# Optimization experiments

Hardware: AMD Instinct MI355X
Metric: run time of the kernel (lower is better)

The kernel has to match this reference:

```python
import jax, jax.numpy as jnp
import numpy as np

N_NODES = 50000
NEG_SLOPE = 0.2

def _gat_conv(x, W, att_src, att_dst, bias, src, dst):
    # x: [N, in_c] -> h: [N, out_c]
    h = x @ W
    a_src = (h * att_src).sum(-1)  # [N]
    a_dst = (h * att_dst).sum(-1)  # [N]
    e = a_src[src] + a_dst[dst]    # [E]
    e = jnp.where(e > 0, e, NEG_SLOPE * e)  # LeakyReLU
    # segment softmax over destination node neighborhoods
    emax = jax.ops.segment_max(e, dst, num_segments=N_NODES)
    ee = jnp.exp(e - emax[dst])
    denom = jax.ops.segment_sum(ee, dst, num_segments=N_NODES)
    alpha = ee / denom[dst]        # [E]
    out = jax.ops.segment_sum(h[src] * alpha[:, None], dst, num_segments=N_NODES)
    return out + bias

def _with_self_loops(edge_index):
    # PyG GATConv default add_self_loops=True
    loop = jnp.arange(N_NODES, dtype=edge_index.dtype)
    src = jnp.concatenate([edge_index[0], loop])
    dst = jnp.concatenate([edge_index[1], loop])
    return src, dst

def setup_inputs() -> dict:
    key = jax.random.key(0)
    ks = jax.random.split(key, 11)
    in_c, hid_c, out_c = 256, 128, 64
    E = 800000
    x = jax.random.normal(ks[0], (N_NODES, in_c), dtype=jnp.float32)
    edge_index = jax.random.randint(ks[1], (2, E), 0, N_NODES, dtype=jnp.int64)
    s1 = 1.0 / np.sqrt(in_c)
    s2 = 1.0 / np.sqrt(hid_c)
    return {
        "x": x,
        "edge_index": edge_index,
        "W1": jax.random.normal(ks[2], (in_c, hid_c), dtype=jnp.float32) * s1,
        "att_src1": jax.random.normal(ks[3], (hid_c,), dtype=jnp.float32) * s2,
        "att_dst1": jax.random.normal(ks[4], (hid_c,), dtype=jnp.float32) * s2,
        "b1": jax.random.normal(ks[5], (hid_c,), dtype=jnp.float32) * 0.01,
        "W2": jax.random.normal(ks[6], (hid_c, out_c), dtype=jnp.float32) * s2,
        "att_src2": jax.random.normal(ks[7], (out_c,), dtype=jnp.float32) * (1.0 / np.sqrt(out_c)),
        "att_dst2": jax.random.normal(ks[8], (out_c,), dtype=jnp.float32) * (1.0 / np.sqrt(out_c)),
        "b2": jax.random.normal(ks[9], (out_c,), dtype=jnp.float32) * 0.01,
    }

def reference(x, edge_index, W1, att_src1, att_dst1, b1, W2, att_src2, att_dst2, b2):
    src, dst = _with_self_loops(edge_index)
    hid = _gat_conv(x, W1, att_src1, att_dst1, b1, src, dst)
    hid = jax.nn.relu(hid)
    out = _gat_conv(hid, W2, att_src2, att_dst2, b2, src, dst)
    return jax.nn.log_softmax(out, axis=1)
```

## Files before the change

kernel.cpp:

```cpp
#include <hip/hip_runtime.h>
#include <hip/hip_bf16.h>
#include <math.h>

#define N_NODES 50000
#define E_RAW   800000
#define E_TOT   850000
#define NEG_SLOPE 0.2f
#define CAP 64

#define NBKT   196
#define BCAP   5376
#define SCHUNK 4096
#define SB     208

typedef __attribute__((ext_vector_type(8))) short short8;
typedef __attribute__((ext_vector_type(4))) float f32x4;

__device__ __forceinline__ short f2bf(float f) {
    __hip_bfloat16 h = __float2bfloat16(f);
    return *reinterpret_cast<short*>(&h);
}
__device__ __forceinline__ unsigned int f2bfu(float f) {
    __hip_bfloat16 h = __float2bfloat16(f);
    return (unsigned int)*reinterpret_cast<unsigned short*>(&h);
}
__device__ __forceinline__ float bflo(unsigned int u) {
    return __uint_as_float(u << 16);
}
__device__ __forceinline__ float bfhi(unsigned int u) {
    return __uint_as_float(u & 0xffff0000u);
}

template<int K, int N>
__global__ __launch_bounds__(256) void gat_wf_kernel(
        const float* __restrict__ W, short* __restrict__ Wf) {
    constexpr int NT = N / 16;
    const int idx = blockIdx.x * 256 + threadIdx.x;
    if (idx >= K * N) return;
    const int j  = idx & 7;
    const int n  = (idx >> 3) & 15;
    const int q  = (idx >> 7) & 3;
    const int t  = (idx >> 9) % NT;
    const int kc = idx / (512 * NT);
    const int k   = kc * 32 + q * 8 + j;
    const int col = t * 16 + n;
    Wf[idx] = f2bf(W[(size_t)k * N + col]);
}

template<int K, int N, bool BF16_IN>
__device__ __forceinline__ void gemm_att_body(
        const int blk,
        const float* __restrict__ xf, const short* __restrict__ xb,
        const short* __restrict__ Wf,
        const float* __restrict__ att_src, const float* __restrict__ att_dst,
        short* __restrict__ h_bf,
        float* __restrict__ a_src, float* __restrict__ a_dst) {
    constexpr int NT = N / 16;
    constexpr int KC = K / 32;
    const int tid  = threadIdx.x;
    const int lane = tid & 63;
    const int wv   = tid >> 6;
    const int mrow = lane & 15;
    const int q    = lane >> 4;

    const int row0 = blk * 64 + wv * 16;
    const int rowA = row0 + mrow;
    const int rowAc = rowA < N_NODES ? rowA : 0;

    f32x4 acc[NT];
    #pragma unroll
    for (int t = 0; t < NT; ++t) acc[t] = f32x4{0.f, 0.f, 0.f, 0.f};

    #pragma unroll
    for (int kc = 0; kc < KC; ++kc) {
        short8 a;
        if (BF16_IN) {
            a = *(const short8*)&xb[(size_t)rowAc * K + kc * 32 + q * 8];
        } else {
            const float4 f0 = *(const float4*)&xf[(size_t)rowAc * K + kc * 32 + q * 8];
            const float4 f1 = *(const float4*)&xf[(size_t)rowAc * K + kc * 32 + q * 8 + 4];
            a[0] = f2bf(f0.x); a[1] = f2bf(f0.y); a[2] = f2bf(f0.z); a[3] = f2bf(f0.w);
            a[4] = f2bf(f1.x); a[5] = f2bf(f1.y); a[6] = f2bf(f1.z); a[7] = f2bf(f1.w);
        }
        #pragma unroll
        for (int t = 0; t < NT; ++t) {
            const short8 b = *(const short8*)&Wf[((size_t)(kc * NT + t) * 64 + lane) * 8];
            acc[t] = __builtin_amdgcn_mfma_f32_16x16x32_bf16(a, b, acc[t], 0, 0, 0);
        }
    }

    #pragma unroll
    for (int r = 0; r < 4; ++r) {
        const int rowD = row0 + q * 4 + r;
        float ps = 0.0f, pd = 0.0f;
        #pragma unroll
        for (int t = 0; t < NT; ++t) {
            const int col = t * 16 + mrow;
            ps = fmaf(acc[t][r], att_src[col], ps);
            pd = fmaf(acc[t][r], att_dst[col], pd);
        }
        #pragma unroll
        for (int off = 8; off > 0; off >>= 1) {
            ps += __shfl_xor(ps, off);
            pd += __shfl_xor(pd, off);
        }
        if (rowD < N_NODES) {
            if (mrow == 0) { a_src[rowD] = ps; a_dst[rowD] = pd; }
            #pragma unroll
            for (int t = 0; t < NT; ++t)
                h_bf[(size_t)rowD * N + t * 16 + mrow] = f2bf(acc[t][r]);
        }
    }
}

template<int K, int N>
__global__ __launch_bounds__(256) void gat_fat1_kernel(
        const float* __restrict__ xf, const short* __restrict__ Wf,
        const float* __restrict__ att_src, const float* __restrict__ att_dst,
        short* __restrict__ h_bf,
        float* __restrict__ a_src, float* __restrict__ a_dst,
        const int* __restrict__ ei, int* __restrict__ gcnt,
        unsigned int* __restrict__ buf, int GB) {
    __shared__ int hist[NBKT];
    __shared__ int base[NBKT];
    if ((int)blockIdx.x < GB) {
        gemm_att_body<K, N, false>(blockIdx.x, xf, nullptr, Wf,
                                   att_src, att_dst, h_bf, a_src, a_dst);
    } else {
        const int sb = (int)blockIdx.x - GB;
        const int c0 = sb * SCHUNK;
        const int c1 = (c0 + SCHUNK < E_TOT) ? c0 + SCHUNK : E_TOT;
        for (int t = threadIdx.x; t < NBKT; t += 256) hist[t] = 0;
        __syncthreads();
        for (int i = c0 + threadIdx.x; i < c1; i += 256) {
            const int d = (i < E_RAW) ? ei[E_RAW + i] : (i - E_RAW);
            atomicAdd(&hist[d >> 8], 1);
        }
        __syncthreads();
        for (int t = threadIdx.x; t < NBKT; t += 256)
            base[t] = atomicAdd(&gcnt[t], hist[t]);
        __syncthreads();
        for (int t = threadIdx.x; t < NBKT; t += 256) hist[t] = 0;
        __syncthreads();
        for (int i = c0 + threadIdx.x; i < c1; i += 256) {
            int s, d;
            if (i < E_RAW) { s = ei[i]; d = ei[E_RAW + i]; }
            else           { s = d = i - E_RAW; }
            const int b = d >> 8;
            const int p = base[b] + atomicAdd(&hist[b], 1);
            if (p < BCAP)
                buf[(size_t)b * BCAP + p] =
                    ((unsigned int)s << 8) | (unsigned int)(d & 255);
        }
    }
}

__global__ __launch_bounds__(256) void gat_ell_kernel(
        const unsigned int* __restrict__ buf, const int* __restrict__ gcnt,
        int* __restrict__ cnt, unsigned short* __restrict__ srcs) {
    const int b = blockIdx.x;
    __shared__ unsigned int c2[256];
    c2[threadIdx.x] = 0;
    __syncthreads();
    int n = gcnt[b];
    n = n < BCAP ? n : BCAP;
    const unsigned int* bb = buf + (size_t)b * BCAP;
    for (int i = threadIdx.x; i < n; i += 256) {
        const unsigned int e = bb[i];
        const int dl = (int)(e & 255u);
        const unsigned int s = e >> 8;
        const unsigned int c = atomicAdd(&c2[dl], 1u);
        if (c < CAP)
            srcs[((size_t)((b << 8) + dl) << 6) + c] = (unsigned short)s;
    }
    __syncthreads();
    const int d = (b << 8) + threadIdx.x;
    if (d < N_NODES) {
        unsigned int c = c2[threadIdx.x];
        cnt[d] = (int)(c < CAP ? c : CAP);
    }
}

template<int K, int N, bool BF16_IN>
__global__ __launch_bounds__(256) void gat_gemm_att_kernel(
        const float* __restrict__ xf, const short* __restrict__ xb,
        const short* __restrict__ Wf,
        const float* __restrict__ att_src, const float* __restrict__ att_dst,
        short* __restrict__ h_bf,
        float* __restrict__ a_src, float* __restrict__ a_dst) {
    gemm_att_body<K, N, BF16_IN>(blockIdx.x, xf, xb, Wf,
                                 att_src, att_dst, h_bf, a_src, a_dst);
}

template<int N, bool RELU, bool LSM, bool OUT_BF16>
__global__ __launch_bounds__(256) void gat_aggr_kernel(
        const int* __restrict__ cnt, const unsigned short* __restrict__ srcs,
        const float* __restrict__ a_src, const float* __restrict__ a_dst,
        const unsigned short* __restrict__ h_bf, const float* __restrict__ bias,
        float* __restrict__ outf, uint4* __restrict__ outb) {
    constexpr int EPL = N / 16;
    const int lane = threadIdx.x & 63;
    const int wave = threadIdx.x >> 6;
    const int d = blockIdx.x * 4 + wave;
    if (d >= N_NODES) return;
    const int beg = d << 6;
    int deg = cnt[d];
    deg = deg < CAP ? deg : CAP;
    const float ad = a_dst[d];

    const int sreg = (int)srcs[beg + (lane < deg ? lane : 0)];
    float e;
    if (lane < deg) {
        float t = a_src[sreg] + ad;
        e = t > 0.0f ? t : NEG_SLOPE * t;
    } else {
        e = -1e30f;
    }
    float m = e;
    #pragma unroll
    for (int off = 32; off > 0; off >>= 1) m = fmaxf(m, __shfl_xor(m, off));
    const float anum = __expf(e - m);
    float ss = anum;
    #pragma unroll
    for (int off = 32; off > 0; off >>= 1) ss += __shfl_xor(ss, off);
    const float areg = anum / ss;

    const int g   = lane >> 4;
    const int sub = lane & 15;
    float acc[EPL];
    #pragma unroll
    for (int c = 0; c < EPL; ++c) acc[c] = 0.0f;

    for (int j = 0; j < deg; j += 4) {
        const int eidx = j + g;
        const int s    = __shfl(sreg, eidx);
        float alpha    = __shfl(areg, eidx);
        if (eidx >= deg) alpha = 0.0f;
        const unsigned short* hp = h_bf + (size_t)s * N + sub * EPL;
        if (EPL == 8) {
            const uint4 hv = *(const uint4*)hp;
            acc[0] = fmaf(alpha, bflo(hv.x), acc[0]);
            acc[1] = fmaf(alpha, bfhi(hv.x), acc[1]);
            acc[2] = fmaf(alpha, bflo(hv.y), acc[2]);
            acc[3] = fmaf(alpha, bfhi(hv.y), acc[3]);
            acc[4] = fmaf(alpha, bflo(hv.z), acc[4]);
            acc[5] = fmaf(alpha, bfhi(hv.z), acc[5]);
            acc[6] = fmaf(alpha, bflo(hv.w), acc[6]);
            acc[7] = fmaf(alpha, bfhi(hv.w), acc[7]);
        } else {
            const uint2 hv = *(const uint2*)hp;
            acc[0] = fmaf(alpha, bflo(hv.x), acc[0]);
            acc[1] = fmaf(alpha, bfhi(hv.x), acc[1]);
            acc[2] = fmaf(alpha, bflo(hv.y), acc[2]);
            acc[3] = fmaf(alpha, bfhi(hv.y), acc[3]);
        }
    }

    #pragma unroll
    for (int c = 0; c < EPL; ++c) {
        acc[c] += __shfl_xor(acc[c], 16);
        acc[c] += __shfl_xor(acc[c], 32);
    }

    if (LSM) {
        float v[4];
        #pragma unroll
        for (int c = 0; c < 4; ++c) v[c] = acc[c] + bias[sub * 4 + c];
        float mm = fmaxf(fmaxf(v[0], v[1]), fmaxf(v[2], v[3]));
        #pragma unroll
        for (int off = 1; off < 16; off <<= 1) mm = fmaxf(mm, __shfl_xor(mm, off));
        float es = __expf(v[0] - mm) + __expf(v[1] - mm)
                 + __expf(v[2] - mm) + __expf(v[3] - mm);
        #pragma unroll
        for (int off = 1; off < 16; off <<= 1) es += __shfl_xor(es, off);
        const float ls = logf(es);
        if (lane < 16) {
            float4 o;
            o.x = v[0] - mm - ls; o.y = v[1] - mm - ls;
            o.z = v[2] - mm - ls; o.w = v[3] - mm - ls;
            *(float4*)&outf[(size_t)d * N + sub * 4] = o;
        }
    } else {
        if (lane < 16) {
            const float4 b0 = *(const float4*)&bias[sub * 8];
            const float4 b1 = *(const float4*)&bias[sub * 8 + 4];
            float v[8];
            v[0] = acc[0] + b0.x; v[1] = acc[1] + b0.y;
            v[2] = acc[2] + b0.z; v[3] = acc[3] + b0.w;
            v[4] = acc[4] + b1.x; v[5] = acc[5] + b1.y;
            v[6] = acc[6] + b1.z; v[7] = acc[7] + b1.w;
            if (RELU)
                #pragma unroll
                for (int c = 0; c < 8; ++c) v[c] = fmaxf(v[c], 0.0f);
            uint4 p;
            p.x = f2bfu(v[0]) | (f2bfu(v[1]) << 16);
            p.y = f2bfu(v[2]) | (f2bfu(v[3]) << 16);
            p.z = f2bfu(v[4]) | (f2bfu(v[5]) << 16);
            p.w = f2bfu(v[6]) | (f2bfu(v[7]) << 16);
            outb[(size_t)d * (N / 8) + sub] = p;
        }
    }
}

extern "C" void kernel_launch(void* const* d_in, const int* in_sizes, int n_in,
                              void* d_out, int out_size, void* d_ws, size_t ws_size,
                              hipStream_t stream) {
    const float* x        = (const float*)d_in[0];
    const int*   ei       = (const int*)  d_in[1];
    const float* W1       = (const float*)d_in[2];
    const float* att_src1 = (const float*)d_in[3];
    const float* att_dst1 = (const float*)d_in[4];
    const float* b1       = (const float*)d_in[5];
    const float* W2       = (const float*)d_in[6];
    const float* att_src2 = (const float*)d_in[7];
    const float* att_dst2 = (const float*)d_in[8];
    const float* b2       = (const float*)d_in[9];
    float* out = (float*)d_out;
    float* ws  = (float*)d_ws;

    float* a_src1 = ws;
    float* a_dst1 = a_src1 + 50000;
    float* a_src2 = a_dst1 + 50000;
    float* a_dst2 = a_src2 + 50000;
    int*   cnt    = (int*)(a_dst2 + 50000);
    int*   gcnt   = cnt + 50000;
    unsigned int*   buf  = (unsigned int*)(gcnt + 256);
    unsigned short* srcs = (unsigned short*)(buf + (size_t)NBKT * BCAP);
    short* hbf1   = (short*)(srcs + (size_t)N_NODES * CAP);
    short* agg1b  = hbf1  + 6400000;
    short* Wf1    = agg1b + 6400000;
    short* Wf2    = Wf1   + 32768;
    short* hbf2   = hbf1;

    hipMemsetAsync(gcnt, 0, NBKT * sizeof(int), stream);

    const int GB = (N_NODES + 63) / 64;

    gat_wf_kernel<256, 128><<<128, 256, 0, stream>>>(W1, Wf1);
    gat_wf_kernel<128, 64><<<32, 256, 0, stream>>>(W2, Wf2);

    gat_fat1_kernel<256, 128><<<GB + SB, 256, 0, stream>>>(
        x, Wf1, att_src1, att_dst1, hbf1, a_src1, a_dst1,
        ei, gcnt, buf, GB);

    gat_ell_kernel<<<NBKT, 256, 0, stream>>>(buf, gcnt, cnt, srcs);

    gat_aggr_kernel<128, true, false, true><<<12500, 256, 0, stream>>>(
        cnt, srcs, a_src1, a_dst1, (const unsigned short*)hbf1, b1,
        nullptr, (uint4*)agg1b);

    gat_gemm_att_kernel<128, 64, true><<<GB, 256, 0, stream>>>(
        nullptr, agg1b, Wf2, att_src2, att_dst2, hbf2, a_src2, a_dst2);
    gat_aggr_kernel<64, false, true, false><<<12500, 256, 0, stream>>>(
        cnt, srcs, a_src2, a_dst2, (const unsigned short*)hbf2, b2,
        out, nullptr);
}
```

Before: 229.0 us.

## Halve bucket width in edge binning and widen per-lane feature chunks in aggregation

The edge bucketing now uses 128-node buckets (392 buckets, smaller per-bucket capacity), so the ELL build kernel launches twice as many blocks, each with 128 local counters. The aggregation kernel now gives each lane twice as many features: 8 edges are processed per iteration with 8 lanes per edge, which raises memory-level parallelism per gather and needs one extra cross-lane reduction step. The log-softmax and bf16 output epilogues are rewritten to match the new lane mapping. Risks are more registers per lane, more idle lanes in the epilogue, and overflow of the smaller bucket capacity if the degree distribution is skewed.

```diff
diff --git a/kernel.cpp b/kernel.cpp
--- a/kernel.cpp
+++ b/kernel.cpp
@@ -8,8 +8,8 @@
 #define NEG_SLOPE 0.2f
 #define CAP 64
 
-#define NBKT   196
-#define BCAP   5376
+#define NBKT   392
+#define BCAP   2944
 #define SCHUNK 4096
 #define SB     208
 
@@ -134,7 +134,7 @@
         __syncthreads();
         for (int i = c0 + threadIdx.x; i < c1; i += 256) {
             const int d = (i < E_RAW) ? ei[E_RAW + i] : (i - E_RAW);
-            atomicAdd(&hist[d >> 8], 1);
+            atomicAdd(&hist[d >> 7], 1);
         }
         __syncthreads();
         for (int t = threadIdx.x; t < NBKT; t += 256)
@@ -146,11 +146,11 @@
             int s, d;
             if (i < E_RAW) { s = ei[i]; d = ei[E_RAW + i]; }
             else           { s = d = i - E_RAW; }
-            const int b = d >> 8;
+            const int b = d >> 7;
             const int p = base[b] + atomicAdd(&hist[b], 1);
             if (p < BCAP)
                 buf[(size_t)b * BCAP + p] =
-                    ((unsigned int)s << 8) | (unsigned int)(d & 255);
+                    ((unsigned int)s << 7) | (unsigned int)(d & 127);
         }
     }
 }
@@ -159,23 +159,23 @@
         const unsigned int* __restrict__ buf, const int* __restrict__ gcnt,
         int* __restrict__ cnt, unsigned short* __restrict__ srcs) {
     const int b = blockIdx.x;
-    __shared__ unsigned int c2[256];
-    c2[threadIdx.x] = 0;
+    __shared__ unsigned int c2[128];
+    if (threadIdx.x < 128) c2[threadIdx.x] = 0;
     __syncthreads();
     int n = gcnt[b];
     n = n < BCAP ? n : BCAP;
     const unsigned int* bb = buf + (size_t)b * BCAP;
     for (int i = threadIdx.x; i < n; i += 256) {
         const unsigned int e = bb[i];
-        const int dl = (int)(e & 255u);
-        const unsigned int s = e >> 8;
+        const int dl = (int)(e & 127u);
+        const unsigned int s = e >> 7;
         const unsigned int c = atomicAdd(&c2[dl], 1u);
         if (c < CAP)
-            srcs[((size_t)((b << 8) + dl) << 6) + c] = (unsigned short)s;
+            srcs[((size_t)((b << 7) + dl) << 6) + c] = (unsigned short)s;
     }
     __syncthreads();
-    const int d = (b << 8) + threadIdx.x;
-    if (d < N_NODES) {
+    const int d = (b << 7) + threadIdx.x;
+    if (threadIdx.x < 128 && d < N_NODES) {
         unsigned int c = c2[threadIdx.x];
         cnt[d] = (int)(c < CAP ? c : CAP);
     }
@@ -192,13 +192,13 @@
                                  att_src, att_dst, h_bf, a_src, a_dst);
 }
 
-template<int N, bool RELU, bool LSM, bool OUT_BF16>
+template<int N, bool RELU, bool LSM>
 __global__ __launch_bounds__(256) void gat_aggr_kernel(
         const int* __restrict__ cnt, const unsigned short* __restrict__ srcs,
         const float* __restrict__ a_src, const float* __restrict__ a_dst,
         const unsigned short* __restrict__ h_bf, const float* __restrict__ bias,
         float* __restrict__ outf, uint4* __restrict__ outb) {
-    constexpr int EPL = N / 16;
+    constexpr int EPL = N / 8;
     const int lane = threadIdx.x & 63;
     const int wave = threadIdx.x >> 6;
     const int d = blockIdx.x * 4 + wave;
@@ -225,79 +225,106 @@
     for (int off = 32; off > 0; off >>= 1) ss += __shfl_xor(ss, off);
     const float areg = anum / ss;
 
-    const int g   = lane >> 4;
-    const int sub = lane & 15;
+    const int g   = lane >> 3;
+    const int sub = lane & 7;
     float acc[EPL];
     #pragma unroll
     for (int c = 0; c < EPL; ++c) acc[c] = 0.0f;
 
-    for (int j = 0; j < deg; j += 4) {
+    for (int j = 0; j < deg; j += 8) {
         const int eidx = j + g;
         const int s    = __shfl(sreg, eidx);
         float alpha    = __shfl(areg, eidx);
         if (eidx >= deg) alpha = 0.0f;
         const unsigned short* hp = h_bf + (size_t)s * N + sub * EPL;
-        if (EPL == 8) {
-            const uint4 hv = *(const uint4*)hp;
-            acc[0] = fmaf(alpha, bflo(hv.x), acc[0]);
-            acc[1] = fmaf(alpha, bfhi(hv.x), acc[1]);
-            acc[2] = fmaf(alpha, bflo(hv.y), acc[2]);
-            acc[3] = fmaf(alpha, bfhi(hv.y), acc[3]);
-            acc[4] = fmaf(alpha, bflo(hv.z), acc[4]);
-            acc[5] = fmaf(alpha, bfhi(hv.z), acc[5]);
-            acc[6] = fmaf(alpha, bflo(hv.w), acc[6]);
-            acc[7] = fmaf(alpha, bfhi(hv.w), acc[7]);
+        if (EPL == 16) {
+            const uint4 h0 = *(const uint4*)hp;
+            const uint4 h1 = *(const uint4*)(hp + 8);
+            acc[0]  = fmaf(alpha, bflo(h0.x), acc[0]);
+            acc[1]  = fmaf(alpha, bfhi(h0.x), acc[1]);
+            acc[2]  = fmaf(alpha, bflo(h0.y), acc[2]);
+            acc[3]  = fmaf(alpha, bfhi(h0.y), acc[3]);
+            acc[4]  = fmaf(alpha, bflo(h0.z), acc[4]);
+            acc[5]  = fmaf(alpha, bfhi(h0.z), acc[5]);
+            acc[6]  = fmaf(alpha, bflo(h0.w), acc[6]);
+            acc[7]  = fmaf(alpha, bfhi(h0.w), acc[7]);
+            acc[8]  = fmaf(alpha, bflo(h1.x), acc[8]);
+            acc[9]  = fmaf(alpha, bfhi(h1.x), acc[9]);
+            acc[10] = fmaf(alpha, bflo(h1.y), acc[10]);
+            acc[11] = fmaf(alpha, bfhi(h1.y), acc[11]);
+            acc[12] = fmaf(alpha, bflo(h1.z), acc[12]);
+            acc[13] = fmaf(alpha, bfhi(h1.z), acc[13]);
+            acc[14] = fmaf(alpha, bflo(h1.w), acc[14]);
+            acc[15] = fmaf(alpha, bfhi(h1.w), acc[15]);
         } else {
-            const uint2 hv = *(const uint2*)hp;
-            acc[0] = fmaf(alpha, bflo(hv.x), acc[0]);
-            acc[1] = fmaf(alpha, bfhi(hv.x), acc[1]);
-            acc[2] = fmaf(alpha, bflo(hv.y), acc[2]);
-            acc[3] = fmaf(alpha, bfhi(hv.y), acc[3]);
+            const uint4 h0 = *(const uint4*)hp;
+            acc[0] = fmaf(alpha, bflo(h0.x), acc[0]);
+            acc[1] = fmaf(alpha, bfhi(h0.x), acc[1]);
+            acc[2] = fmaf(alpha, bflo(h0.y), acc[2]);
+            acc[3] = fmaf(alpha, bfhi(h0.y), acc[3]);
+            acc[4] = fmaf(alpha, bflo(h0.z), acc[4]);
+            acc[5] = fmaf(alpha, bfhi(h0.z), acc[5]);
+            acc[6] = fmaf(alpha, bflo(h0.w), acc[6]);
+            acc[7] = fmaf(alpha, bfhi(h0.w), acc[7]);
         }
     }
 
     #pragma unroll
     for (int c = 0; c < EPL; ++c) {
+        acc[c] += __shfl_xor(acc[c], 8);
         acc[c] += __shfl_xor(acc[c], 16);
         acc[c] += __shfl_xor(acc[c], 32);
     }
 
     if (LSM) {
-        float v[4];
-        #pragma unroll
-        for (int c = 0; c < 4; ++c) v[c] = acc[c] + bias[sub * 4 + c];
-        float mm = fmaxf(fmaxf(v[0], v[1]), fmaxf(v[2], v[3]));
-        #pragma unroll
-        for (int off = 1; off < 16; off <<= 1) mm = fmaxf(mm, __shfl_xor(mm, off));
-        float es = __expf(v[0] - mm) + __expf(v[1] - mm)
-                 + __expf(v[2] - mm) + __expf(v[3] - mm);
-        #pragma unroll
-        for (int off = 1; off < 16; off <<= 1) es += __shfl_xor(es, off);
+        float v[8];
+        #pragma unroll
+        for (int c = 0; c < 8; ++c) v[c] = acc[c] + bias[sub * 8 + c];
+        float mm = v[0];
+        #pragma unroll
+        for (int c = 1; c < 8; ++c) mm = fmaxf(mm, v[c]);
+        #pragma unroll
+        for (int off = 1; off < 8; off <<= 1) mm = fmaxf(mm, __shfl_xor(mm, off));
+        float es = 0.0f;
+        #pragma unroll
+        for (int c = 0; c < 8; ++c) es += __expf(v[c] - mm);
+        #pragma unroll
+        for (int off = 1; off < 8; off <<= 1) es += __shfl_xor(es, off);
         const float ls = logf(es);
-        if (lane < 16) {
-            float4 o;
-            o.x = v[0] - mm - ls; o.y = v[1] - mm - ls;
-            o.z = v[2] - mm - ls; o.w = v[3] - mm - ls;
-            *(float4*)&outf[(size_t)d * N + sub * 4] = o;
+        if (lane < 8) {
+            float4 o0, o1;
+            o0.x = v[0] - mm - ls; o0.y = v[1] - mm - ls;
+            o0.z = v[2] - mm - ls; o0.w = v[3] - mm - ls;
+            o1.x = v[4] - mm - ls; o1.y = v[5] - mm - ls;
+            o1.z = v[6] - mm - ls; o1.w = v[7] - mm - ls;
+            *(float4*)&outf[(size_t)d * N + sub * 8]     = o0;
+            *(float4*)&outf[(size_t)d * N + sub * 8 + 4] = o1;
         }
     } else {
-        if (lane < 16) {
-            const float4 b0 = *(const float4*)&bias[sub * 8];
-            const float4 b1 = *(const float4*)&bias[sub * 8 + 4];
-            float v[8];
-            v[0] = acc[0] + b0.x; v[1] = acc[1] + b0.y;
-            v[2] = acc[2] + b0.z; v[3] = acc[3] + b0.w;
-            v[4] = acc[4] + b1.x; v[5] = acc[5] + b1.y;
-            v[6] = acc[6] + b1.z; v[7] = acc[7] + b1.w;
+        if (lane < 8) {
+            float v[16];
+            #pragma unroll
+            for (int c = 0; c < 16; c += 4) {
+                const float4 bb = *(const float4*)&bias[sub * 16 + c];
+                v[c]   = acc[c]   + bb.x;
+                v[c+1] = acc[c+1] + bb.y;
+                v[c+2] = acc[c+2] + bb.z;
+                v[c+3] = acc[c+3] + bb.w;
+            }
             if (RELU)
                 #pragma unroll
-                for (int c = 0; c < 8; ++c) v[c] = fmaxf(v[c], 0.0f);
-            uint4 p;
-            p.x = f2bfu(v[0]) | (f2bfu(v[1]) << 16);
-            p.y = f2bfu(v[2]) | (f2bfu(v[3]) << 16);
-            p.z = f2bfu(v[4]) | (f2bfu(v[5]) << 16);
-            p.w = f2bfu(v[6]) | (f2bfu(v[7]) << 16);
-            outb[(size_t)d * (N / 8) + sub] = p;
+                for (int c = 0; c < 16; ++c) v[c] = fmaxf(v[c], 0.0f);
+            uint4 p0, p1;
+            p0.x = f2bfu(v[0])  | (f2bfu(v[1])  << 16);
+            p0.y = f2bfu(v[2])  | (f2bfu(v[3])  << 16);
+            p0.z = f2bfu(v[4])  | (f2bfu(v[5])  << 16);
+            p0.w = f2bfu(v[6])  | (f2bfu(v[7])  << 16);
+            p1.x = f2bfu(v[8])  | (f2bfu(v[9])  << 16);
+            p1.y = f2bfu(v[10]) | (f2bfu(v[11]) << 16);
+            p1.z = f2bfu(v[12]) | (f2bfu(v[13]) << 16);
+            p1.w = f2bfu(v[14]) | (f2bfu(v[15]) << 16);
+            outb[(size_t)d * (N / 8) + sub * 2]     = p0;
+            outb[(size_t)d * (N / 8) + sub * 2 + 1] = p1;
         }
     }
 }
@@ -324,7 +351,7 @@
     float* a_dst2 = a_src2 + 50000;
     int*   cnt    = (int*)(a_dst2 + 50000);
     int*   gcnt   = cnt + 50000;
-    unsigned int*   buf  = (unsigned int*)(gcnt + 256);
+    unsigned int*   buf  = (unsigned int*)(gcnt + 512);
     unsigned short* srcs = (unsigned short*)(buf + (size_t)NBKT * BCAP);
     short* hbf1   = (short*)(srcs + (size_t)N_NODES * CAP);
     short* agg1b  = hbf1  + 6400000;
@@ -345,13 +372,13 @@
 
     gat_ell_kernel<<<NBKT, 256, 0, stream>>>(buf, gcnt, cnt, srcs);
 
-    gat_aggr_kernel<128, true, false, true><<<12500, 256, 0, stream>>>(
+    gat_aggr_kernel<128, true, false><<<12500, 256, 0, stream>>>(
         cnt, srcs, a_src1, a_dst1, (const unsigned short*)hbf1, b1,
         nullptr, (uint4*)agg1b);
 
     gat_gemm_att_kernel<128, 64, true><<<GB, 256, 0, stream>>>(
         nullptr, agg1b, Wf2, att_src2, att_dst2, hbf2, a_src2, a_dst2);
-    gat_aggr_kernel<64, false, true, false><<<12500, 256, 0, stream>>>(
+    gat_aggr_kernel<64, false, true><<<12500, 256, 0, stream>>>(
         cnt, srcs, a_src2, a_dst2, (const unsigned short*)hbf2, b2,
         out, nullptr);
 }
```

Result: no change. 225.9 us (-1.3%).
